# Optimization experiments

Measured on AMD Instinct MI355X. Metric: run time of the kernel, lower is better.

## Reference

```python
import jax, jax.numpy as jnp
import numpy as np

S, N, M, D = 4, 4096, 4096, 128
NEG = -1e30
EPS = 1e-12


def setup_inputs() -> dict:
    key = jax.random.key(0)
    k1, k2, k3 = jax.random.split(key, 3)
    art = jax.random.normal(k1, (S, N, D), dtype=jnp.float32)
    ref = jax.random.normal(k2, (S, M, D), dtype=jnp.float32)
    pos_mask = jax.random.randint(k3, (S, N, M), 0, 2).astype(jnp.bool_)
    log_temperature = jnp.log(jnp.asarray(0.01, dtype=jnp.float32))
    return {"art": art, "ref": ref, "pos_mask": pos_mask, "log_temperature": log_temperature}


def _l2norm(x):
    # F.normalize: x / max(||x||, eps)
    n = jnp.sqrt(jnp.sum(x * x, axis=-1, keepdims=True))
    return x / jnp.maximum(n, EPS)


def reference(art, ref, pos_mask, log_temperature):
    temp = jnp.exp(log_temperature)
    a = _l2norm(art)                                   # [S,N,D]
    r = _l2norm(ref)                                   # [S,M,D]
    logits = jnp.einsum("snd,smd->snm", a, r) / temp   # [S,N,M]

    den = jax.nn.logsumexp(logits, axis=-1)                              # [S,N]
    num = jax.nn.logsumexp(jnp.where(pos_mask, logits, NEG), axis=-1)    # [S,N]

    n_pos = jnp.sum(pos_mask, axis=-1)                 # [S,N]
    n_ref = logits.shape[-1]
    valid = (n_pos > 0) & (n_ref > n_pos)              # skip anchors with 0 pos or all pos

    per_anchor = den - num                             # -(num - den)
    cnt = jnp.sum(valid, axis=-1)                      # [S]
    stem_loss = jnp.sum(jnp.where(valid, per_anchor, 0.0), axis=-1) / jnp.maximum(cnt, 1)
    stem_valid = cnt > 0
    loss = jnp.sum(jnp.where(stem_valid, stem_loss, 0.0)) / jnp.maximum(jnp.sum(stem_valid), 1)
    return loss
```

## Files before the change

### kernel.cpp

```cpp
#include <hip/hip_runtime.h>
#include <hip/hip_bf16.h>
#include <math.h>

#define S_ 4
#define N_ 4096
#define M_ 4096
#define D_ 128
#define NEG_ (-1e30f)
#define CH_ 2
#define MCH_ (M_ / CH_)
#define NST_ (MCH_ / 64)
#define LN2_ 0.69314718055994531f
#define LOG2E_ 1.44269504088896340f
#define NWORDS_ (S_ * N_ * (M_ / 16))

typedef __bf16 bf16x8 __attribute__((ext_vector_type(8)));
typedef float f32x4 __attribute__((ext_vector_type(4)));

__device__ __forceinline__ void gll16(const void* g, void* l) {
    __builtin_amdgcn_global_load_lds(
        (const __attribute__((address_space(1))) unsigned int*)g,
        (__attribute__((address_space(3))) unsigned int*)l, 16, 0, 0);
}

__device__ __forceinline__ unsigned short f2bf(float f) {
    unsigned u = __float_as_uint(f);
    unsigned r = (u + 0x7FFFu + ((u >> 16) & 1u)) >> 16;
    return (unsigned short)r;
}

__global__ void nrm_rows_kernel(const float* __restrict__ art, const float* __restrict__ ref,
                                unsigned short* __restrict__ an, unsigned short* __restrict__ rn) {
    const int w = threadIdx.x >> 6;
    const int lane = threadIdx.x & 63;
    const int row = blockIdx.x * 4 + w;
    const bool is_art = row < S_ * N_;
    const float* src = is_art ? (art + (size_t)row * D_)
                              : (ref + (size_t)(row - S_ * N_) * D_);
    unsigned short* dst = is_art ? (an + (size_t)row * D_)
                                 : (rn + (size_t)(row - S_ * N_) * D_);
    const float2 v = *reinterpret_cast<const float2*>(src + lane * 2);
    float ss = v.x * v.x + v.y * v.y;
#pragma unroll
    for (int off = 1; off < 64; off <<= 1) ss += __shfl_xor(ss, off);
    const float scale = 1.0f / fmaxf(sqrtf(ss), 1e-12f);
    unsigned pack = (unsigned)f2bf(v.x * scale) | ((unsigned)f2bf(v.y * scale) << 16);
    *reinterpret_cast<unsigned*>(dst + lane * 2) = pack;
}

__global__ __launch_bounds__(256) void bitpack_kernel(const unsigned* __restrict__ maskp,
                                                      unsigned short* __restrict__ bits) {
    const unsigned probe = maskp[threadIdx.x & 63];
    const bool byte_mode = (__ballot(probe > 1u) != 0ull);
    const int stride = gridDim.x * 256;
    const int4* p = (const int4*)maskp;
    if (byte_mode) {
        for (int i = blockIdx.x * 256 + threadIdx.x; i < NWORDS_; i += stride) {
            const int4 q = p[i];
            unsigned v =  ((unsigned)q.x & 1u)         | ((((unsigned)q.x >> 8) & 1u) << 1)
                       | ((((unsigned)q.x >> 16) & 1u) << 2) | ((((unsigned)q.x >> 24) & 1u) << 3)
                       | (((unsigned)q.y & 1u) << 4)   | ((((unsigned)q.y >> 8) & 1u) << 5)
                       | ((((unsigned)q.y >> 16) & 1u) << 6) | ((((unsigned)q.y >> 24) & 1u) << 7)
                       | (((unsigned)q.z & 1u) << 8)   | ((((unsigned)q.z >> 8) & 1u) << 9)
                       | ((((unsigned)q.z >> 16) & 1u) << 10) | ((((unsigned)q.z >> 24) & 1u) << 11)
                       | (((unsigned)q.w & 1u) << 12)  | ((((unsigned)q.w >> 8) & 1u) << 13)
                       | ((((unsigned)q.w >> 16) & 1u) << 14) | ((((unsigned)q.w >> 24) & 1u) << 15);
            bits[i] = (unsigned short)v;
        }
    } else {
        for (int i = blockIdx.x * 256 + threadIdx.x; i < NWORDS_; i += stride) {
            const int4 a = p[i * 4 + 0], b = p[i * 4 + 1], c = p[i * 4 + 2], d = p[i * 4 + 3];
            unsigned v =  ((unsigned)a.x & 1u)        | (((unsigned)a.y & 1u) << 1)
                       | (((unsigned)a.z & 1u) << 2)  | (((unsigned)a.w & 1u) << 3)
                       | (((unsigned)b.x & 1u) << 4)  | (((unsigned)b.y & 1u) << 5)
                       | (((unsigned)b.z & 1u) << 6)  | (((unsigned)b.w & 1u) << 7)
                       | (((unsigned)c.x & 1u) << 8)  | (((unsigned)c.y & 1u) << 9)
                       | (((unsigned)c.z & 1u) << 10) | (((unsigned)c.w & 1u) << 11)
                       | (((unsigned)d.x & 1u) << 12) | (((unsigned)d.y & 1u) << 13)
                       | (((unsigned)d.z & 1u) << 14) | (((unsigned)d.w & 1u) << 15);
            bits[i] = (unsigned short)v;
        }
    }
}

__global__ __launch_bounds__(256, 4) void infonce_main_kernel(
    const unsigned short* __restrict__ an, const unsigned short* __restrict__ rn,
    const unsigned* __restrict__ bits32, const float* __restrict__ logtemp,
    float4* __restrict__ part4) {

    const int bid = blockIdx.x;
    const int swz = (bid & 7) * 128 + (bid >> 3);
    const int ch = swz >> 9;
    const int s = (swz >> 7) & 3;
    const int nblk = swz & 127;
    const int n_base = nblk * 32;

    const int tid = threadIdx.x;
    const int w = tid >> 6;
    const int lane = tid & 63;
    const int nsub = w & 1;
    const int msub = w >> 1;
    const int n16 = n_base + nsub * 16;
    const int lrow = lane & 15;
    const int lgrp = lane >> 4;
    const float scale2 = __expf(-logtemp[0]) * LOG2E_;

    __shared__ unsigned char smem[2][64 * 256];
    __shared__ float4 lds4[4][16];

    bf16x8 bfr[4];
    const unsigned short* abase = an + ((size_t)(s * N_ + n16 + lrow)) * D_ + lgrp * 8;
#pragma unroll
    for (int kc = 0; kc < 4; ++kc)
        bfr[kc] = *reinterpret_cast<const bf16x8*>(abase + kc * 32);

    const int srow = w * 4 + (lane >> 4);
    const int schunk = (lane & 15) ^ (srow & 7);
    const int lane_src_off = srow * 256 + schunk * 16;
    const unsigned char* rn_chunk =
        (const unsigned char*)(rn + ((size_t)(s * M_ + ch * MCH_)) * D_);

    const unsigned* bw = bits32 + (size_t)(s * N_ + n16 + lrow) * (M_ / 32) + ch * (MCH_ / 32) + msub;

    const int rb0 = (msub * 32 + lrow) * 256;
    int coff[4];
#pragma unroll
    for (int kc = 0; kc < 4; ++kc) coff[kc] = ((kc * 4 + lgrp) ^ (lrow & 7)) * 16;

    float dmax = NEG_, dsum = 0.f, nsum = 0.f;
    int npos = 0;

    {
        const unsigned char* src = rn_chunk + lane_src_off;
        unsigned char* dst = &smem[0][w * 1024];
#pragma unroll
        for (int j = 0; j < 4; ++j) gll16(src + j * 4096, dst + j * 4096);
    }
    __syncthreads();

    for (int st = 0; st < NST_; ++st) {
        const int nb = st & 1;
        if (st + 1 < NST_) {
            const unsigned char* src = rn_chunk + (size_t)(st + 1) * 16384 + lane_src_off;
            unsigned char* dst = &smem[nb ^ 1][w * 1024];
#pragma unroll
            for (int j = 0; j < 4; ++j) gll16(src + j * 4096, dst + j * 4096);
        }
        const unsigned w32 = bw[st * 2];
        const unsigned char* base = &smem[nb][0] + rb0;
        f32x4 acc0 = {0.f, 0.f, 0.f, 0.f}, acc1 = {0.f, 0.f, 0.f, 0.f};
#pragma unroll
        for (int kc = 0; kc < 4; ++kc) {
            acc0 = __builtin_amdgcn_mfma_f32_16x16x32_bf16(
                *reinterpret_cast<const bf16x8*>(base + coff[kc]), bfr[kc], acc0, 0, 0, 0);
            acc1 = __builtin_amdgcn_mfma_f32_16x16x32_bf16(
                *reinterpret_cast<const bf16x8*>(base + 4096 + coff[kc]), bfr[kc], acc1, 0, 0, 0);
        }
        float l0 = acc0[0] * scale2, l1 = acc0[1] * scale2, l2 = acc0[2] * scale2, l3 = acc0[3] * scale2;
        float l4 = acc1[0] * scale2, l5 = acc1[1] * scale2, l6 = acc1[2] * scale2, l7 = acc1[3] * scale2;
        float tmax = fmaxf(fmaxf(fmaxf(l0, l1), fmaxf(l2, l3)),
                           fmaxf(fmaxf(l4, l5), fmaxf(l6, l7)));
        const float nmx = fmaxf(dmax, tmax);
        const float r = exp2f(dmax - nmx);
        float e0 = exp2f(l0 - nmx), e1 = exp2f(l1 - nmx), e2 = exp2f(l2 - nmx), e3 = exp2f(l3 - nmx);
        float e4 = exp2f(l4 - nmx), e5 = exp2f(l5 - nmx), e6 = exp2f(l6 - nmx), e7 = exp2f(l7 - nmx);
        dsum = dsum * r + (((e0 + e1) + (e2 + e3)) + ((e4 + e5) + (e6 + e7)));
        const unsigned nib0 = (w32 >> (lgrp * 4)) & 0xFu;
        const unsigned nib1 = (w32 >> (16 + lgrp * 4)) & 0xFu;
        float p0 = ((nib0 & 1u) ? e0 : 0.f) + (((nib0 >> 1) & 1u) ? e1 : 0.f);
        float p1 = (((nib0 >> 2) & 1u) ? e2 : 0.f) + (((nib0 >> 3) & 1u) ? e3 : 0.f);
        float p2 = ((nib1 & 1u) ? e4 : 0.f) + (((nib1 >> 1) & 1u) ? e5 : 0.f);
        float p3 = (((nib1 >> 2) & 1u) ? e6 : 0.f) + (((nib1 >> 3) & 1u) ? e7 : 0.f);
        nsum = nsum * r + ((p0 + p1) + (p2 + p3));
        npos += __popc(nib0 | (nib1 << 4));
        dmax = nmx;
        __syncthreads();
    }

    float npf = (float)npos;
#pragma unroll
    for (int off = 16; off < 64; off <<= 1) {
        float odm = __shfl_xor(dmax, off), ods = __shfl_xor(dsum, off);
        float ons = __shfl_xor(nsum, off), onp = __shfl_xor(npf, off);
        float nm = fmaxf(dmax, odm);
        float ra = exp2f(dmax - nm), rb = exp2f(odm - nm);
        dsum = dsum * ra + ods * rb;
        nsum = nsum * ra + ons * rb;
        npf += onp;
        dmax = nm;
    }

    if (lane < 16) lds4[w][lane] = make_float4(dmax, dsum, nsum, npf);
    __syncthreads();

    if (w == 0 && lane < 32) {
        const int wsub = lane >> 4;
        const int ni = lane & 15;
        const float4 A = lds4[wsub][ni];
        const float4 B = lds4[wsub + 2][ni];
        const float nm = fmaxf(A.x, B.x);
        const float ra = exp2f(A.x - nm), rb = exp2f(B.x - nm);
        const float ds = A.y * ra + B.y * rb;
        const float ns = A.z * ra + B.z * rb;
        const float np = A.w + B.w;
        const int ag = s * N_ + n_base + wsub * 16 + ni;
        part4[ag * CH_ + ch] = make_float4(nm, ds, ns, np);
    }
}

__global__ void reduce_kernel(const float4* __restrict__ part4, float2* __restrict__ bpart) {
    const int a = blockIdx.x * 256 + threadIdx.x;
    const int w = threadIdx.x >> 6;
    const int lane = threadIdx.x & 63;
    float dm = NEG_, ds = 0.f, ns = 0.f, npf = 0.f;
#pragma unroll
    for (int ch = 0; ch < CH_; ++ch) {
        const float4 p = part4[a * CH_ + ch];
        const float m2 = fmaxf(dm, p.x);
        const float ra = exp2f(dm - m2), rb = exp2f(p.x - m2);
        ds = ds * ra + p.y * rb;
        ns = ns * ra + p.z * rb;
        npf += p.w;
        dm = m2;
    }
    const bool valid = (npf > 0.5f) && (npf < (float)M_ - 0.5f);
    float pa = valid ? LN2_ * (log2f(ds) - log2f(ns)) : 0.f;
    float cv = valid ? 1.f : 0.f;
#pragma unroll
    for (int off = 1; off < 64; off <<= 1) {
        pa += __shfl_xor(pa, off);
        cv += __shfl_xor(cv, off);
    }
    __shared__ float sp[4], sc[4];
    if (lane == 0) { sp[w] = pa; sc[w] = cv; }
    __syncthreads();
    if (threadIdx.x == 0)
        bpart[blockIdx.x] = make_float2(sp[0] + sp[1] + sp[2] + sp[3],
                                        sc[0] + sc[1] + sc[2] + sc[3]);
}

__global__ void finalize_kernel(const float2* __restrict__ bpart, float* __restrict__ out) {
    const int t = threadIdx.x;
    const float2 v = bpart[t];
    float pa = v.x, cv = v.y;
#pragma unroll
    for (int off = 1; off < 16; off <<= 1) {
        pa += __shfl_xor(pa, off);
        cv += __shfl_xor(cv, off);
    }
    const float p0 = __shfl(pa, 0),  c0 = __shfl(cv, 0);
    const float p1 = __shfl(pa, 16), c1 = __shfl(cv, 16);
    const float p2 = __shfl(pa, 32), c2 = __shfl(cv, 32);
    const float p3 = __shfl(pa, 48), c3 = __shfl(cv, 48);
    if (t == 0) {
        float total = 0.f;
        int scnt = 0;
        const float ps[4] = {p0, p1, p2, p3};
        const float cs[4] = {c0, c1, c2, c3};
        for (int s = 0; s < S_; ++s) {
            const float stem = ps[s] / fmaxf(cs[s], 1.f);
            if (cs[s] > 0.f) { total += stem; scnt++; }
        }
        out[0] = total / (float)(scnt > 0 ? scnt : 1);
    }
}

extern "C" void kernel_launch(void* const* d_in, const int* in_sizes, int n_in,
                              void* d_out, int out_size, void* d_ws, size_t ws_size,
                              hipStream_t stream) {
    const float* art = (const float*)d_in[0];
    const float* ref = (const float*)d_in[1];
    const void* mask = d_in[2];
    const float* lt = (const float*)d_in[3];
    float* out = (float*)d_out;

    char* ws = (char*)d_ws;
    unsigned short* an = (unsigned short*)ws;
    unsigned short* rn = (unsigned short*)(ws + (size_t)4194304);
    unsigned short* bits = (unsigned short*)(ws + (size_t)8388608);
    float4* part4 = (float4*)(ws + (size_t)16777216);
    float2* bpart = (float2*)(ws + (size_t)17825792);

    nrm_rows_kernel<<<(S_ * (N_ + M_)) / 4, 256, 0, stream>>>(art, ref, an, rn);
    bitpack_kernel<<<4096, 256, 0, stream>>>((const unsigned*)mask, bits);
    infonce_main_kernel<<<S_ * (N_ / 32) * CH_, 256, 0, stream>>>(
        an, rn, (const unsigned*)bits, lt, part4);
    reduce_kernel<<<(S_ * N_) / 256, 256, 0, stream>>>(part4, bpart);
    finalize_kernel<<<1, 64, 0, stream>>>(bpart, out);
}
```

Before: 430.3 us.

## Fuse mask bit-packing into main kernel via prefetched ballots into shared memory

Removes the separate bitpack kernel and its round trip through workspace. The main kernel now reads the boolean mask bytes directly, one byte per lane per row, and packs them with wavefront ballots into a double-buffered shared array. Mask loads for the next tile are issued alongside the next reference-tile prefetch. This saves one launch and the packed-bits write and read, but it adds narrow byte-sized global loads, eight ballots per step, and a byte/int mode probe in every block.

Result: faster. 409.9 us (-4.7%).

```diff
diff --git a/kernel.cpp b/kernel.cpp
--- a/kernel.cpp
+++ b/kernel.cpp
@@ -12,7 +12,6 @@
 #define NST_ (MCH_ / 64)
 #define LN2_ 0.69314718055994531f
 #define LOG2E_ 1.44269504088896340f
-#define NWORDS_ (S_ * N_ * (M_ / 16))
 
 typedef __bf16 bf16x8 __attribute__((ext_vector_type(8)));
 typedef float f32x4 __attribute__((ext_vector_type(4)));
@@ -48,44 +47,9 @@
     *reinterpret_cast<unsigned*>(dst + lane * 2) = pack;
 }
 
-__global__ __launch_bounds__(256) void bitpack_kernel(const unsigned* __restrict__ maskp,
-                                                      unsigned short* __restrict__ bits) {
-    const unsigned probe = maskp[threadIdx.x & 63];
-    const bool byte_mode = (__ballot(probe > 1u) != 0ull);
-    const int stride = gridDim.x * 256;
-    const int4* p = (const int4*)maskp;
-    if (byte_mode) {
-        for (int i = blockIdx.x * 256 + threadIdx.x; i < NWORDS_; i += stride) {
-            const int4 q = p[i];
-            unsigned v =  ((unsigned)q.x & 1u)         | ((((unsigned)q.x >> 8) & 1u) << 1)
-                       | ((((unsigned)q.x >> 16) & 1u) << 2) | ((((unsigned)q.x >> 24) & 1u) << 3)
-                       | (((unsigned)q.y & 1u) << 4)   | ((((unsigned)q.y >> 8) & 1u) << 5)
-                       | ((((unsigned)q.y >> 16) & 1u) << 6) | ((((unsigned)q.y >> 24) & 1u) << 7)
-                       | (((unsigned)q.z & 1u) << 8)   | ((((unsigned)q.z >> 8) & 1u) << 9)
-                       | ((((unsigned)q.z >> 16) & 1u) << 10) | ((((unsigned)q.z >> 24) & 1u) << 11)
-                       | (((unsigned)q.w & 1u) << 12)  | ((((unsigned)q.w >> 8) & 1u) << 13)
-                       | ((((unsigned)q.w >> 16) & 1u) << 14) | ((((unsigned)q.w >> 24) & 1u) << 15);
-            bits[i] = (unsigned short)v;
-        }
-    } else {
-        for (int i = blockIdx.x * 256 + threadIdx.x; i < NWORDS_; i += stride) {
-            const int4 a = p[i * 4 + 0], b = p[i * 4 + 1], c = p[i * 4 + 2], d = p[i * 4 + 3];
-            unsigned v =  ((unsigned)a.x & 1u)        | (((unsigned)a.y & 1u) << 1)
-                       | (((unsigned)a.z & 1u) << 2)  | (((unsigned)a.w & 1u) << 3)
-                       | (((unsigned)b.x & 1u) << 4)  | (((unsigned)b.y & 1u) << 5)
-                       | (((unsigned)b.z & 1u) << 6)  | (((unsigned)b.w & 1u) << 7)
-                       | (((unsigned)c.x & 1u) << 8)  | (((unsigned)c.y & 1u) << 9)
-                       | (((unsigned)c.z & 1u) << 10) | (((unsigned)c.w & 1u) << 11)
-                       | (((unsigned)d.x & 1u) << 12) | (((unsigned)d.y & 1u) << 13)
-                       | (((unsigned)d.z & 1u) << 14) | (((unsigned)d.w & 1u) << 15);
-            bits[i] = (unsigned short)v;
-        }
-    }
-}
-
 __global__ __launch_bounds__(256, 4) void infonce_main_kernel(
     const unsigned short* __restrict__ an, const unsigned short* __restrict__ rn,
-    const unsigned* __restrict__ bits32, const float* __restrict__ logtemp,
+    const unsigned char* __restrict__ maskb, const float* __restrict__ logtemp,
     float4* __restrict__ part4) {
 
     const int bid = blockIdx.x;
@@ -105,7 +69,15 @@
     const int lgrp = lane >> 4;
     const float scale2 = __expf(-logtemp[0]) * LOG2E_;
 
+    const unsigned* mu = (const unsigned*)maskb;
+    unsigned pr = 0;
+#pragma unroll
+    for (int i = 0; i < 4; ++i) pr |= (mu[i * 64 + lane] > 1u) ? 1u : 0u;
+    const bool byte_mode = (__ballot(pr != 0) != 0ull);
+    const size_t mstride = byte_mode ? 1 : 4;
+
     __shared__ unsigned char smem[2][64 * 256];
+    __shared__ unsigned long long mbuf[2][32];
     __shared__ float4 lds4[4][16];
 
     bf16x8 bfr[4];
@@ -120,7 +92,10 @@
     const unsigned char* rn_chunk =
         (const unsigned char*)(rn + ((size_t)(s * M_ + ch * MCH_)) * D_);
 
-    const unsigned* bw = bits32 + (size_t)(s * N_ + n16 + lrow) * (M_ / 32) + ch * (MCH_ / 32) + msub;
+    size_t rowb[8];
+#pragma unroll
+    for (int r = 0; r < 8; ++r)
+        rowb[r] = ((size_t)(s * N_ + n_base + w * 8 + r) * M_ + (size_t)ch * MCH_) * mstride;
 
     const int rb0 = (msub * 32 + lrow) * 256;
     int coff[4];
@@ -135,18 +110,33 @@
         unsigned char* dst = &smem[0][w * 1024];
 #pragma unroll
         for (int j = 0; j < 4; ++j) gll16(src + j * 4096, dst + j * 4096);
+        unsigned char mv[8];
+        const size_t eoff = (size_t)lane * mstride;
+#pragma unroll
+        for (int r = 0; r < 8; ++r) mv[r] = maskb[rowb[r] + eoff];
+        unsigned long long bl[8];
+#pragma unroll
+        for (int r = 0; r < 8; ++r) bl[r] = __ballot(mv[r] != 0);
+        if (lane == 0) {
+#pragma unroll
+            for (int r = 0; r < 8; ++r) mbuf[0][w * 8 + r] = bl[r];
+        }
     }
     __syncthreads();
 
     for (int st = 0; st < NST_; ++st) {
         const int nb = st & 1;
-        if (st + 1 < NST_) {
+        const bool pf = (st + 1 < NST_);
+        unsigned char mv[8];
+        if (pf) {
             const unsigned char* src = rn_chunk + (size_t)(st + 1) * 16384 + lane_src_off;
             unsigned char* dst = &smem[nb ^ 1][w * 1024];
 #pragma unroll
             for (int j = 0; j < 4; ++j) gll16(src + j * 4096, dst + j * 4096);
-        }
-        const unsigned w32 = bw[st * 2];
+            const size_t eoff = (size_t)((st + 1) * 64 + lane) * mstride;
+#pragma unroll
+            for (int r = 0; r < 8; ++r) mv[r] = maskb[rowb[r] + eoff];
+        }
         const unsigned char* base = &smem[nb][0] + rb0;
         f32x4 acc0 = {0.f, 0.f, 0.f, 0.f}, acc1 = {0.f, 0.f, 0.f, 0.f};
 #pragma unroll
@@ -156,6 +146,9 @@
             acc1 = __builtin_amdgcn_mfma_f32_16x16x32_bf16(
                 *reinterpret_cast<const bf16x8*>(base + 4096 + coff[kc]), bfr[kc], acc1, 0, 0, 0);
         }
+        const unsigned long long wmask = mbuf[nb][nsub * 16 + lrow];
+        const unsigned nib0 = (unsigned)(wmask >> (msub * 32 + lgrp * 4)) & 0xFu;
+        const unsigned nib1 = (unsigned)(wmask >> (msub * 32 + 16 + lgrp * 4)) & 0xFu;
         float l0 = acc0[0] * scale2, l1 = acc0[1] * scale2, l2 = acc0[2] * scale2, l3 = acc0[3] * scale2;
         float l4 = acc1[0] * scale2, l5 = acc1[1] * scale2, l6 = acc1[2] * scale2, l7 = acc1[3] * scale2;
         float tmax = fmaxf(fmaxf(fmaxf(l0, l1), fmaxf(l2, l3)),
@@ -165,8 +158,6 @@
         float e0 = exp2f(l0 - nmx), e1 = exp2f(l1 - nmx), e2 = exp2f(l2 - nmx), e3 = exp2f(l3 - nmx);
         float e4 = exp2f(l4 - nmx), e5 = exp2f(l5 - nmx), e6 = exp2f(l6 - nmx), e7 = exp2f(l7 - nmx);
         dsum = dsum * r + (((e0 + e1) + (e2 + e3)) + ((e4 + e5) + (e6 + e7)));
-        const unsigned nib0 = (w32 >> (lgrp * 4)) & 0xFu;
-        const unsigned nib1 = (w32 >> (16 + lgrp * 4)) & 0xFu;
         float p0 = ((nib0 & 1u) ? e0 : 0.f) + (((nib0 >> 1) & 1u) ? e1 : 0.f);
         float p1 = (((nib0 >> 2) & 1u) ? e2 : 0.f) + (((nib0 >> 3) & 1u) ? e3 : 0.f);
         float p2 = ((nib1 & 1u) ? e4 : 0.f) + (((nib1 >> 1) & 1u) ? e5 : 0.f);
@@ -174,6 +165,15 @@
         nsum = nsum * r + ((p0 + p1) + (p2 + p3));
         npos += __popc(nib0 | (nib1 << 4));
         dmax = nmx;
+        if (pf) {
+            unsigned long long bl[8];
+#pragma unroll
+            for (int r2 = 0; r2 < 8; ++r2) bl[r2] = __ballot(mv[r2] != 0);
+            if (lane == 0) {
+#pragma unroll
+                for (int r2 = 0; r2 < 8; ++r2) mbuf[nb ^ 1][w * 8 + r2] = bl[r2];
+            }
+        }
         __syncthreads();
     }
 
@@ -270,21 +270,18 @@
                               hipStream_t stream) {
     const float* art = (const float*)d_in[0];
     const float* ref = (const float*)d_in[1];
-    const void* mask = d_in[2];
+    const unsigned char* mask = (const unsigned char*)d_in[2];
     const float* lt = (const float*)d_in[3];
     float* out = (float*)d_out;
 
     char* ws = (char*)d_ws;
     unsigned short* an = (unsigned short*)ws;
     unsigned short* rn = (unsigned short*)(ws + (size_t)4194304);
-    unsigned short* bits = (unsigned short*)(ws + (size_t)8388608);
-    float4* part4 = (float4*)(ws + (size_t)16777216);
-    float2* bpart = (float2*)(ws + (size_t)17825792);
+    float4* part4 = (float4*)(ws + (size_t)8388608);
+    float2* bpart = (float2*)(ws + (size_t)9437184);
 
     nrm_rows_kernel<<<(S_ * (N_ + M_)) / 4, 256, 0, stream>>>(art, ref, an, rn);
-    bitpack_kernel<<<4096, 256, 0, stream>>>((const unsigned*)mask, bits);
-    infonce_main_kernel<<<S_ * (N_ / 32) * CH_, 256, 0, stream>>>(
-        an, rn, (const unsigned*)bits, lt, part4);
+    infonce_main_kernel<<<S_ * (N_ / 32) * CH_, 256, 0, stream>>>(an, rn, mask, lt, part4);
     reduce_kernel<<<(S_ * N_) / 256, 256, 0, stream>>>(part4, bpart);
     finalize_kernel<<<1, 64, 0, stream>>>(bpart, out);
 }
```
